# Kernel optimization log

Hardware: AMD Instinct MI355X
Metric: run time of the kernel (lower is better)

Reference implementation:

```python
import jax, jax.numpy as jnp
import numpy as np

SCALE_SIZE = 1.0
EPS = 1e-5
B, N, C, OUT, W = 32, 4096, 256, 512, 64


def _conv1x1(x, w, b):
    # x: (B, Cin, N), w: (Cout, Cin), b: (Cout,)
    return jnp.einsum('oc,bcn->bon', w, x) + b[:, None]


def _bn(x, g, be, m, v):
    # eval-mode BatchNorm1d over channel dim of (B, C, N)
    return (x - m[:, None]) * (g[:, None] / jnp.sqrt(v[:, None] + EPS)) + be[:, None]


def _bn_params(k, c):
    k1, k2, k3, k4 = jax.random.split(k, 4)
    g = jax.random.uniform(k1, (c,)) * 0.5 + 0.75
    be = jax.random.normal(k2, (c,)) * 0.1
    m = jax.random.normal(k3, (c,)) * 0.1
    v = jax.random.uniform(k4, (c,)) * 0.5 + 0.5
    return g, be, m, v


def setup_inputs() -> dict:
    key = jax.random.key(0)
    ks = jax.random.split(key, 16)
    d = {}
    d['xyz'] = jax.random.normal(ks[0], (B, N, 3), dtype=jnp.float32)
    d['feature'] = jax.random.normal(ks[1], (B, C, N), dtype=jnp.float32)
    d['idx'] = jax.random.randint(ks[2], (B, N), 0, N, dtype=jnp.int64)
    # WeightNet1D: 3 -> 64 -> 64 -> 64
    d['w1'] = jax.random.normal(ks[3], (W, 3), dtype=jnp.float32) * 0.3
    d['b1'] = jax.random.normal(ks[4], (W,), dtype=jnp.float32) * 0.05
    d['g1'], d['be1'], d['m1'], d['v1'] = _bn_params(ks[5], W)
    d['w2'] = jax.random.normal(ks[6], (W, W), dtype=jnp.float32) * 0.1
    d['b2'] = jax.random.normal(ks[7], (W,), dtype=jnp.float32) * 0.05
    d['g2'], d['be2'], d['m2'], d['v2'] = _bn_params(ks[8], W)
    d['w3'] = jax.random.normal(ks[9], (W, W), dtype=jnp.float32) * 0.1
    d['b3'] = jax.random.normal(ks[10], (W,), dtype=jnp.float32) * 0.05
    d['g3'], d['be3'], d['m3'], d['v3'] = _bn_params(ks[11], W)
    # final ConvBNRelu1D: C*W -> OUT, kernel 1
    d['wf'] = jax.random.normal(ks[12], (OUT, C * W), dtype=jnp.float32) * 0.01
    d['bf'] = jax.random.normal(ks[13], (OUT,), dtype=jnp.float32) * 0.05
    d['gf'], d['bef'], d['mf'], d['vf'] = _bn_params(ks[14], OUT)
    return d


def reference(xyz, feature, idx,
              w1, b1, g1, be1, m1, v1,
              w2, b2, g2, be2, m2, v2,
              w3, b3, g3, be3, m3, v3,
              wf, bf, gf, bef, mf, vf):
    # xyz: (B, N, 3) -> (B, 3, N), scaled
    x = jnp.transpose(xyz, (0, 2, 1)) / SCALE_SIZE
    x = jax.nn.relu(_bn(_conv1x1(x, w1, b1), g1, be1, m1, v1))
    x = jax.nn.relu(_bn(_conv1x1(x, w2, b2), g2, be2, m2, v2))
    weights = jax.nn.relu(_bn(_conv1x1(x, w3, b3), g3, be3, m3, v3))
    n = feature.shape[2]
    feat = feature / n
    # (B, C, N) x (B, N, 64) -> (B, C, 64)
    agg = jnp.einsum('bcn,bwn->bcw', feat, weights)
    agg = agg.reshape(agg.shape[0], -1, 1)  # (B, C*64, 1)
    out = jax.nn.relu(_bn(_conv1x1(agg, wf, bf), gf, bef, mf, vf))
    return out  # (B, OUT, 1)
```

## Files before the change

### kernel.cpp

```cpp
#include <hip/hip_runtime.h>
#include <hip/hip_bf16.h>

#define B_ 32
#define N_ 4096
#define C_ 256
#define W_ 64
#define OUT_ 512
#define EPS_ 1e-5f

typedef __attribute__((ext_vector_type(8))) short short8;
typedef __attribute__((ext_vector_type(4))) float floatx4;

#define WT_OFF     0
#define AGGB_OFF   16777216
#define PART_OFF   17825792
#define WS_NEEDED  19922944

#define GLOAD_LDS16(g, l)                                                  \
  __builtin_amdgcn_global_load_lds(                                        \
      (const __attribute__((address_space(1))) void*)(g),                  \
      (__attribute__((address_space(3))) void*)(l), 16, 0, 0)

__device__ __forceinline__ ushort f2bf(float f) {
  unsigned u = __builtin_bit_cast(unsigned, f);
  unsigned r = (u + 0x7fffu + ((u >> 16) & 1u)) >> 16;
  return (ushort)r;
}
__device__ __forceinline__ unsigned pk2(float a, float b) {
  return (unsigned)f2bf(a) | ((unsigned)f2bf(b) << 16);
}

__global__ __launch_bounds__(256) void k1_weightnet(
    const float* __restrict__ xyz,
    const float* __restrict__ w1, const float* __restrict__ b1,
    const float* __restrict__ g1, const float* __restrict__ be1,
    const float* __restrict__ m1, const float* __restrict__ v1,
    const float* __restrict__ w2, const float* __restrict__ b2,
    const float* __restrict__ g2, const float* __restrict__ be2,
    const float* __restrict__ m2, const float* __restrict__ v2,
    const float* __restrict__ w3, const float* __restrict__ b3,
    const float* __restrict__ g3, const float* __restrict__ be3,
    const float* __restrict__ m3, const float* __restrict__ v3,
    ushort* __restrict__ wt) {
  __shared__ __align__(16) ushort h_lds[256 * 72];
  __shared__ __align__(16) ushort w2_lds[64 * 72];
  __shared__ __align__(16) ushort w3_lds[64 * 72];
  __shared__ float w1l[192];
  __shared__ float b1l[64];
  __shared__ float b2_lds[64];
  __shared__ float b3_lds[64];

  const int t = threadIdx.x;
  const int blk = blockIdx.x;
  const int b = blk >> 4;
  const int n0 = (blk & 15) << 8;

  if (t < 64) {
    float s1 = g1[t] * rsqrtf(v1[t] + EPS_);
#pragma unroll
    for (int j = 0; j < 3; ++j) w1l[t * 3 + j] = w1[t * 3 + j] * s1;
    b1l[t] = (b1[t] - m1[t]) * s1 + be1[t];

    float s2 = g2[t] * rsqrtf(v2[t] + EPS_);
    unsigned* w2row = (unsigned*)&w2_lds[t * 72];
#pragma unroll
    for (int q = 0; q < 16; ++q) {
      float4 v = *(const float4*)&w2[t * 64 + q * 4];
      w2row[q * 2] = pk2(v.x * s2, v.y * s2);
      w2row[q * 2 + 1] = pk2(v.z * s2, v.w * s2);
    }
    w2row[32] = 0; w2row[33] = 0; w2row[34] = 0; w2row[35] = 0;
    b2_lds[t] = (b2[t] - m2[t]) * s2 + be2[t];

    float s3 = g3[t] * rsqrtf(v3[t] + EPS_);
    unsigned* w3row = (unsigned*)&w3_lds[t * 72];
#pragma unroll
    for (int q = 0; q < 16; ++q) {
      float4 v = *(const float4*)&w3[t * 64 + q * 4];
      w3row[q * 2] = pk2(v.x * s3, v.y * s3);
      w3row[q * 2 + 1] = pk2(v.z * s3, v.w * s3);
    }
    w3row[32] = 0; w3row[33] = 0; w3row[34] = 0; w3row[35] = 0;
    b3_lds[t] = (b3[t] - m3[t]) * s3 + be3[t];
  }
  __syncthreads();

  const int n = n0 + t;
  const float* xp = xyz + ((size_t)b * N_ + n) * 3;
  float x0 = xp[0], x1 = xp[1], x2 = xp[2];
  unsigned* hrow = (unsigned*)&h_lds[t * 72];
#pragma unroll 4
  for (int cp = 0; cp < 32; ++cp) {
    int c0 = cp * 2, c1 = cp * 2 + 1;
    float a0 = fmaxf(b1l[c0] + w1l[c0 * 3] * x0 + w1l[c0 * 3 + 1] * x1 + w1l[c0 * 3 + 2] * x2, 0.f);
    float a1 = fmaxf(b1l[c1] + w1l[c1 * 3] * x0 + w1l[c1 * 3 + 1] * x1 + w1l[c1 * 3 + 2] * x2, 0.f);
    hrow[cp] = pk2(a0, a1);
  }
  __syncthreads();

  const int wv = t >> 6, lane = t & 63;
  const int lrow = lane & 15, lk = lane >> 4;

  floatx4 acc[4][4];
#pragma unroll
  for (int mt = 0; mt < 4; ++mt)
#pragma unroll
    for (int nt = 0; nt < 4; ++nt) acc[mt][nt] = (floatx4){0.f, 0.f, 0.f, 0.f};

#pragma unroll
  for (int ks = 0; ks < 2; ++ks) {
    short8 afr[4], bfr[4];
#pragma unroll
    for (int mt = 0; mt < 4; ++mt)
      afr[mt] = *(const short8*)&h_lds[(wv * 64 + mt * 16 + lrow) * 72 + ks * 32 + lk * 8];
#pragma unroll
    for (int nt = 0; nt < 4; ++nt)
      bfr[nt] = *(const short8*)&w2_lds[(nt * 16 + lrow) * 72 + ks * 32 + lk * 8];
#pragma unroll
    for (int mt = 0; mt < 4; ++mt)
#pragma unroll
      for (int nt = 0; nt < 4; ++nt)
        acc[mt][nt] = __builtin_amdgcn_mfma_f32_16x16x32_bf16(afr[mt], bfr[nt], acc[mt][nt], 0, 0, 0);
  }
#pragma unroll
  for (int mt = 0; mt < 4; ++mt)
#pragma unroll
    for (int nt = 0; nt < 4; ++nt) {
      float bias = b2_lds[nt * 16 + lrow];
#pragma unroll
      for (int r = 0; r < 4; ++r) {
        float v = fmaxf(acc[mt][nt][r] + bias, 0.f);
        h_lds[(wv * 64 + mt * 16 + lk * 4 + r) * 72 + nt * 16 + lrow] = f2bf(v);
      }
    }

  floatx4 acc3[4][4];
#pragma unroll
  for (int mt = 0; mt < 4; ++mt)
#pragma unroll
    for (int nt = 0; nt < 4; ++nt) acc3[mt][nt] = (floatx4){0.f, 0.f, 0.f, 0.f};

#pragma unroll
  for (int ks = 0; ks < 2; ++ks) {
    short8 afr[4], bfr[4];
#pragma unroll
    for (int mt = 0; mt < 4; ++mt)
      afr[mt] = *(const short8*)&h_lds[(wv * 64 + mt * 16 + lrow) * 72 + ks * 32 + lk * 8];
#pragma unroll
    for (int nt = 0; nt < 4; ++nt)
      bfr[nt] = *(const short8*)&w3_lds[(nt * 16 + lrow) * 72 + ks * 32 + lk * 8];
#pragma unroll
    for (int mt = 0; mt < 4; ++mt)
#pragma unroll
      for (int nt = 0; nt < 4; ++nt)
        acc3[mt][nt] = __builtin_amdgcn_mfma_f32_16x16x32_bf16(afr[mt], bfr[nt], acc3[mt][nt], 0, 0, 0);
  }

  __syncthreads();
  unsigned* T = (unsigned*)h_lds;
#pragma unroll
  for (int mt = 0; mt < 4; ++mt)
#pragma unroll
    for (int nt = 0; nt < 4; ++nt) {
      float bias = b3_lds[nt * 16 + lrow];
      float v0 = fmaxf(acc3[mt][nt][0] + bias, 0.f);
      float v1 = fmaxf(acc3[mt][nt][1] + bias, 0.f);
      float v2 = fmaxf(acc3[mt][nt][2] + bias, 0.f);
      float v3 = fmaxf(acc3[mt][nt][3] + bias, 0.f);
      int ch = nt * 16 + lrow;
      int pp = (wv * 64 + mt * 16 + lk * 4) >> 1;
      T[ch * 132 + pp] = pk2(v0, v1);
      T[ch * 132 + pp + 1] = pk2(v2, v3);
    }
  __syncthreads();

  const int ch = t >> 2, q = t & 3;
  unsigned* wtu = (unsigned*)wt;
  size_t obase = ((size_t)(b * W_ + ch)) * (N_ / 2) + (n0 >> 1);
#pragma unroll
  for (int j = 0; j < 8; ++j) {
    int col = q * 4 + j * 16;
    uint4 vv = *(const uint4*)&T[ch * 132 + col];
    *(uint4*)&wtu[obase + col] = vv;
  }
}

__global__ __launch_bounds__(256) void k2_agg(const float* __restrict__ feature,
                                              const ushort* __restrict__ wt,
                                              ushort* __restrict__ aggB) {
  __shared__ __align__(16) float A_lds[3][32 * 128];
  __shared__ __align__(16) ushort B_lds[3][64 * 128];

  const int t = threadIdx.x;
  const int wv = t >> 6, lane = t & 63;
  const int lrow = lane & 15, lk = lane >> 4;
  const int blk = blockIdx.x;
  const int b = blk & 31;
  const int ct = blk >> 5;

  const float* fbase = feature + (size_t)(b * C_ + ct * 32) * N_;
  const ushort* wbase = wt + (size_t)(b * W_) * N_;

  const int rowA = (lane >> 5);
  const int colA = (lane & 31);
  const int rowB = (lane >> 4);
  const int colB = (lane & 15);

#define STAGE(buf, step)                                                          \
  do {                                                                            \
    _Pragma("unroll")                                                             \
    for (int q = 0; q < 4; ++q) {                                                 \
      int j = wv * 4 + q;                                                         \
      int ra = 2 * j + rowA;                                                      \
      int ga = colA ^ (ra & 7);              \
      GLOAD_LDS16(fbase + (size_t)ra * N_ + (step) * 128 + ga * 4,                \
                  &A_lds[buf][j * 256 + lane * 4]);                               \
      int rb = 4 * j + rowB;                                                      \
      int gb = colB ^ (rb & 7);                                                   \
      GLOAD_LDS16(wbase + (size_t)rb * N_ + (step) * 128 + gb * 8,                \
                  &B_lds[buf][j * 512 + lane * 8]);                               \
    }                                                                             \
  } while (0)

  const int cg = wv >> 1, wg = wv & 1;
  const int r_c = cg * 16 + lrow;
  const int eA = r_c & 7;
  const int r_w0 = wg * 32 + lrow;
  const int eB0 = r_w0 & 7, eB1 = (r_w0 + 16) & 7;

  floatx4 acc[2];
  acc[0] = (floatx4){0.f, 0.f, 0.f, 0.f};
  acc[1] = (floatx4){0.f, 0.f, 0.f, 0.f};

  auto compute = [&](int cur) {
    const float* abuf = &A_lds[cur][r_c * 128];
    const ushort* bbuf0 = &B_lds[cur][r_w0 * 128];
    const ushort* bbuf1 = &B_lds[cur][(r_w0 + 16) * 128];
#pragma unroll
    for (int ksl = 0; ksl < 4; ++ksl) {
      const int p = ksl * 8 + lk * 2;
      float4 fa = *(const float4*)&abuf[((p) ^ eA) * 4];
      float4 fb = *(const float4*)&abuf[((p + 1) ^ eA) * 4];
      union { unsigned u[4]; short8 s8; } pa;
      pa.u[0] = pk2(fa.x, fa.y);
      pa.u[1] = pk2(fa.z, fa.w);
      pa.u[2] = pk2(fb.x, fb.y);
      pa.u[3] = pk2(fb.z, fb.w);
      const int g = ksl * 4 + lk;
      short8 b0 = *(const short8*)&bbuf0[(g ^ eB0) * 8];
      short8 b1 = *(const short8*)&bbuf1[(g ^ eB1) * 8];
      acc[0] = __builtin_amdgcn_mfma_f32_16x16x32_bf16(pa.s8, b0, acc[0], 0, 0, 0);
      acc[1] = __builtin_amdgcn_mfma_f32_16x16x32_bf16(pa.s8, b1, acc[1], 0, 0, 0);
    }
  };

#define WAIT_BAR(n) asm volatile("s_waitcnt vmcnt(" #n ")\n\ts_barrier" ::: "memory")
#define BAR()       asm volatile("s_barrier" ::: "memory")

  STAGE(0, 0);
  STAGE(1, 1);
  for (int g = 0; g < 10; ++g) {
    STAGE(2, 3 * g + 2); WAIT_BAR(16); compute(0); BAR();
    STAGE(0, 3 * g + 3); WAIT_BAR(16); compute(1); BAR();
    STAGE(1, 3 * g + 4); WAIT_BAR(16); compute(2); BAR();
  }
  WAIT_BAR(8);  compute(0); BAR();
  WAIT_BAR(0);  compute(1);
#undef STAGE
#undef WAIT_BAR
#undef BAR

  const float sc = 1.f / 4096.f;
  ushort* dst = aggB + (size_t)b * 16384;
#pragma unroll
  for (int wt2 = 0; wt2 < 2; ++wt2)
#pragma unroll
    for (int r = 0; r < 4; ++r) {
      int c = ct * 32 + cg * 16 + lk * 4 + r;
      int w = wg * 32 + wt2 * 16 + lrow;
      dst[c * 64 + w] = f2bf(acc[wt2][r] * sc);
    }
}

__global__ __launch_bounds__(256) void k3_final(const float* __restrict__ wf,
                                                const ushort* __restrict__ aggB,
                                                float* __restrict__ part) {
  const int t = threadIdx.x;
  const int wv = t >> 6, lane = t & 63;
  const int lrow = lane & 15, lk = lane >> 4;
  const int ot = blockIdx.x >> 5;
  const int kb = blockIdx.x & 31;
  const int o0 = ot * 64 + wv * 16;
  const int k0 = kb * 512;

  const float* wp = wf + (size_t)(o0 + lrow) * 16384 + k0 + lk * 8;
  const ushort* a0 = aggB + (size_t)lrow * 16384 + k0 + lk * 8;
  const ushort* a1 = a0 + (size_t)16 * 16384;

  floatx4 acc0 = {0.f, 0.f, 0.f, 0.f}, acc1 = {0.f, 0.f, 0.f, 0.f};
#pragma unroll 8
  for (int s = 0; s < 16; ++s) {
    float4 f0 = *(const float4*)(wp + s * 32);
    float4 f1 = *(const float4*)(wp + s * 32 + 4);
    short8 b0 = *(const short8*)(a0 + s * 32);
    short8 b1 = *(const short8*)(a1 + s * 32);
    union { unsigned u[4]; short8 s8; } pa;
    pa.u[0] = pk2(f0.x, f0.y);
    pa.u[1] = pk2(f0.z, f0.w);
    pa.u[2] = pk2(f1.x, f1.y);
    pa.u[3] = pk2(f1.z, f1.w);
    acc0 = __builtin_amdgcn_mfma_f32_16x16x32_bf16(pa.s8, b0, acc0, 0, 0, 0);
    acc1 = __builtin_amdgcn_mfma_f32_16x16x32_bf16(pa.s8, b1, acc1, 0, 0, 0);
  }

  float* dst = part + (size_t)kb * 16384;
#pragma unroll
  for (int r = 0; r < 4; ++r) {
    int o = o0 + lk * 4 + r;
    dst[o * 32 + lrow] = acc0[r];
    dst[o * 32 + 16 + lrow] = acc1[r];
  }
}

__global__ __launch_bounds__(64) void k4_finalize(
    const float* __restrict__ bf, const float* __restrict__ gf,
    const float* __restrict__ bef, const float* __restrict__ mf,
    const float* __restrict__ vf, const float* __restrict__ part,
    float* __restrict__ out) {
  int i = blockIdx.x * 64 + threadIdx.x;
  int o = i >> 5, b = i & 31;
  float v = 0.f;
#pragma unroll
  for (int kb = 0; kb < 32; ++kb) v += part[(size_t)kb * 16384 + i];
  float s = gf[o] * rsqrtf(vf[o] + EPS_);
  float r = (v + bf[o] - mf[o]) * s + bef[o];
  out[b * OUT_ + o] = fmaxf(r, 0.f);
}

extern "C" void kernel_launch(void* const* d_in, const int* in_sizes, int n_in,
                              void* d_out, int out_size, void* d_ws, size_t ws_size,
                              hipStream_t stream) {
  const float* xyz     = (const float*)d_in[0];
  const float* feature = (const float*)d_in[1];
  const float* w1 = (const float*)d_in[3];
  const float* b1 = (const float*)d_in[4];
  const float* g1 = (const float*)d_in[5];
  const float* be1 = (const float*)d_in[6];
  const float* m1 = (const float*)d_in[7];
  const float* v1 = (const float*)d_in[8];
  const float* w2 = (const float*)d_in[9];
  const float* b2 = (const float*)d_in[10];
  const float* g2 = (const float*)d_in[11];
  const float* be2 = (const float*)d_in[12];
  const float* m2 = (const float*)d_in[13];
  const float* v2 = (const float*)d_in[14];
  const float* w3 = (const float*)d_in[15];
  const float* b3 = (const float*)d_in[16];
  const float* g3 = (const float*)d_in[17];
  const float* be3 = (const float*)d_in[18];
  const float* m3 = (const float*)d_in[19];
  const float* v3 = (const float*)d_in[20];
  const float* wf = (const float*)d_in[21];
  const float* bf = (const float*)d_in[22];
  const float* gf = (const float*)d_in[23];
  const float* bef = (const float*)d_in[24];
  const float* mf = (const float*)d_in[25];
  const float* vf = (const float*)d_in[26];

  char* ws = (char*)d_ws;
  if (ws_size < (size_t)WS_NEEDED) return;
  ushort* wt   = (ushort*)(ws + WT_OFF);
  ushort* aggB = (ushort*)(ws + AGGB_OFF);
  float*  part = (float*)(ws + PART_OFF);

  k1_weightnet<<<512, 256, 0, stream>>>(xyz,
                                        w1, b1, g1, be1, m1, v1,
                                        w2, b2, g2, be2, m2, v2,
                                        w3, b3, g3, be3, m3, v3, wt);
  k2_agg<<<256, 256, 0, stream>>>(feature, wt, aggB);
  k3_final<<<256, 256, 0, stream>>>(wf, aggB, part);
  k4_finalize<<<256, 64, 0, stream>>>(bf, gf, bef, mf, vf, part, (float*)d_out);
}
```

Measured before the change: 61.22 us.

## Convert feature to bf16 in registers before LDS and double-buffer agg kernel

The aggregation kernel now loads feature rows into registers, converts them to bf16 with a cheaper round-half-up pack, and writes them to LDS in swizzled form. Previously it copied fp32 rows straight into LDS and converted on every MFMA read. The K step grows from 128 to 256 and the pipeline drops from triple to double buffering with a full wait per step. This halves LDS footprint and read traffic for A and removes repeated conversion work. The trade-offs are higher register use and less overlap, because each step waits on vmcnt(0). The final GEMV kernel also switches to the cheaper pk2h rounding, which rounds ties away from zero instead of to nearest even.

```diff
diff --git a/kernel.cpp b/kernel.cpp
--- a/kernel.cpp
+++ b/kernel.cpp
@@ -28,6 +28,11 @@
 }
 __device__ __forceinline__ unsigned pk2(float a, float b) {
   return (unsigned)f2bf(a) | ((unsigned)f2bf(b) << 16);
+}
+__device__ __forceinline__ unsigned pk2h(float a, float b) {
+  unsigned ua = __builtin_bit_cast(unsigned, a);
+  unsigned ub = __builtin_bit_cast(unsigned, b);
+  return ((ua + 0x8000u) >> 16) | ((ub + 0x8000u) & 0xffff0000u);
 }
 
 __global__ __launch_bounds__(256) void k1_weightnet(
@@ -188,98 +193,118 @@
 __global__ __launch_bounds__(256) void k2_agg(const float* __restrict__ feature,
                                               const ushort* __restrict__ wt,
                                               ushort* __restrict__ aggB) {
-  __shared__ __align__(16) float A_lds[3][32 * 128];
-  __shared__ __align__(16) ushort B_lds[3][64 * 128];
+  __shared__ __align__(16) ushort A_lds[2][32 * 256];
+  __shared__ __align__(16) ushort B_lds[2][64 * 256];
 
   const int t = threadIdx.x;
   const int wv = t >> 6, lane = t & 63;
   const int lrow = lane & 15, lk = lane >> 4;
-  const int blk = blockIdx.x;
-  const int b = blk & 31;
-  const int ct = blk >> 5;
+  const int b = blockIdx.x & 31;
+  const int ct = blockIdx.x >> 5;
 
   const float* fbase = feature + (size_t)(b * C_ + ct * 32) * N_;
   const ushort* wbase = wt + (size_t)(b * W_) * N_;
 
-  const int rowA = (lane >> 5);
-  const int colA = (lane & 31);
-  const int rowB = (lane >> 4);
-  const int colB = (lane & 15);
-
-#define STAGE(buf, step)                                                          \
-  do {                                                                            \
-    _Pragma("unroll")                                                             \
-    for (int q = 0; q < 4; ++q) {                                                 \
-      int j = wv * 4 + q;                                                         \
-      int ra = 2 * j + rowA;                                                      \
-      int ga = colA ^ (ra & 7);              \
-      GLOAD_LDS16(fbase + (size_t)ra * N_ + (step) * 128 + ga * 4,                \
-                  &A_lds[buf][j * 256 + lane * 4]);                               \
-      int rb = 4 * j + rowB;                                                      \
-      int gb = colB ^ (rb & 7);                                                   \
-      GLOAD_LDS16(wbase + (size_t)rb * N_ + (step) * 128 + gb * 8,                \
-                  &B_lds[buf][j * 512 + lane * 8]);                               \
-    }                                                                             \
+  const int aj = wv * 8 + (lane >> 3);
+  const int ac = (lane & 7) * 32;
+  const float* fsrc = fbase + (size_t)aj * N_ + ac;
+  const int eAW = aj & 7;
+
+  const int brh = lane >> 5;
+  const int bgr = lane & 31;
+
+  float4 areg[8];
+
+#define A_ISSUE(step)                                                        \
+  do {                                                                       \
+    _Pragma("unroll")                                                        \
+    for (int q = 0; q < 8; ++q)                                              \
+      areg[q] = *(const float4*)(fsrc + (size_t)(step) * 256 + q * 4);       \
   } while (0)
 
+#define A_WRITE(buf)                                                         \
+  do {                                                                       \
+    ushort* drow = &A_lds[buf][aj * 256];                                    \
+    _Pragma("unroll")                                                        \
+    for (int w = 0; w < 4; ++w) {                                            \
+      uint4 d;                                                               \
+      d.x = pk2h(areg[w * 2].x, areg[w * 2].y);                              \
+      d.y = pk2h(areg[w * 2].z, areg[w * 2].w);                              \
+      d.z = pk2h(areg[w * 2 + 1].x, areg[w * 2 + 1].y);                      \
+      d.w = pk2h(areg[w * 2 + 1].z, areg[w * 2 + 1].w);                      \
+      int g = ((lane & 7) * 4 + w) ^ eAW;                                    \
+      *(uint4*)(drow + g * 8) = d;                                           \
+    }                                                                        \
+  } while (0)
+
+#define B_STAGE(buf, step)                                                   \
+  do {                                                                       \
+    _Pragma("unroll")                                                        \
+    for (int j2 = 0; j2 < 8; ++j2) {                                         \
+      int row = wv * 16 + 2 * j2 + brh;                                      \
+      int sg = bgr ^ (row & 7);                                              \
+      GLOAD_LDS16(wbase + (size_t)row * N_ + (step) * 256 + sg * 8,          \
+                  &B_lds[buf][(wv * 16 + 2 * j2) * 256 + lane * 8]);         \
+    }                                                                        \
+  } while (0)
+
   const int cg = wv >> 1, wg = wv & 1;
-  const int r_c = cg * 16 + lrow;
-  const int eA = r_c & 7;
-  const int r_w0 = wg * 32 + lrow;
-  const int eB0 = r_w0 & 7, eB1 = (r_w0 + 16) & 7;
-
-  floatx4 acc[2];
-  acc[0] = (floatx4){0.f, 0.f, 0.f, 0.f};
-  acc[1] = (floatx4){0.f, 0.f, 0.f, 0.f};
-
-  auto compute = [&](int cur) {
-    const float* abuf = &A_lds[cur][r_c * 128];
-    const ushort* bbuf0 = &B_lds[cur][r_w0 * 128];
-    const ushort* bbuf1 = &B_lds[cur][(r_w0 + 16) * 128];
-#pragma unroll
-    for (int ksl = 0; ksl < 4; ++ksl) {
-      const int p = ksl * 8 + lk * 2;
-      float4 fa = *(const float4*)&abuf[((p) ^ eA) * 4];
-      float4 fb = *(const float4*)&abuf[((p + 1) ^ eA) * 4];
-      union { unsigned u[4]; short8 s8; } pa;
-      pa.u[0] = pk2(fa.x, fa.y);
-      pa.u[1] = pk2(fa.z, fa.w);
-      pa.u[2] = pk2(fb.x, fb.y);
-      pa.u[3] = pk2(fb.z, fb.w);
-      const int g = ksl * 4 + lk;
-      short8 b0 = *(const short8*)&bbuf0[(g ^ eB0) * 8];
-      short8 b1 = *(const short8*)&bbuf1[(g ^ eB1) * 8];
-      acc[0] = __builtin_amdgcn_mfma_f32_16x16x32_bf16(pa.s8, b0, acc[0], 0, 0, 0);
-      acc[1] = __builtin_amdgcn_mfma_f32_16x16x32_bf16(pa.s8, b1, acc[1], 0, 0, 0);
-    }
-  };
-
-#define WAIT_BAR(n) asm volatile("s_waitcnt vmcnt(" #n ")\n\ts_barrier" ::: "memory")
-#define BAR()       asm volatile("s_barrier" ::: "memory")
-
-  STAGE(0, 0);
-  STAGE(1, 1);
-  for (int g = 0; g < 10; ++g) {
-    STAGE(2, 3 * g + 2); WAIT_BAR(16); compute(0); BAR();
-    STAGE(0, 3 * g + 3); WAIT_BAR(16); compute(1); BAR();
-    STAGE(1, 3 * g + 4); WAIT_BAR(16); compute(2); BAR();
-  }
-  WAIT_BAR(8);  compute(0); BAR();
-  WAIT_BAR(0);  compute(1);
-#undef STAGE
-#undef WAIT_BAR
-#undef BAR
+  const int rA = cg * 16 + lrow, eA = rA & 7;
+  const int rB0 = wg * 32 + lrow, eB0 = rB0 & 7;
+  const int rB1 = rB0 + 16, eB1 = rB1 & 7;
+
+  floatx4 acc0 = {0.f, 0.f, 0.f, 0.f}, acc1 = {0.f, 0.f, 0.f, 0.f};
+
+#define COMPUTE(buf)                                                         \
+  do {                                                                       \
+    const ushort* Ab = &A_lds[buf][rA * 256];                                \
+    const ushort* Bb0 = &B_lds[buf][rB0 * 256];                              \
+    const ushort* Bb1 = &B_lds[buf][rB1 * 256];                              \
+    _Pragma("unroll")                                                        \
+    for (int ksl = 0; ksl < 8; ++ksl) {                                      \
+      int g = ksl * 4 + lk;                                                  \
+      short8 a = *(const short8*)(Ab + (g ^ eA) * 8);                        \
+      short8 b0 = *(const short8*)(Bb0 + (g ^ eB0) * 8);                     \
+      short8 b1 = *(const short8*)(Bb1 + (g ^ eB1) * 8);                     \
+      acc0 = __builtin_amdgcn_mfma_f32_16x16x32_bf16(a, b0, acc0, 0, 0, 0);  \
+      acc1 = __builtin_amdgcn_mfma_f32_16x16x32_bf16(a, b1, acc1, 0, 0, 0);  \
+    }                                                                        \
+  } while (0)
+
+#define SYNC_STEP() asm volatile("s_waitcnt vmcnt(0) lgkmcnt(0)\n\ts_barrier" ::: "memory")
+
+  A_ISSUE(0); B_STAGE(0, 0);
+  A_WRITE(0);
+  A_ISSUE(1); B_STAGE(1, 1);
+  asm volatile("s_waitcnt vmcnt(16) lgkmcnt(0)\n\ts_barrier" ::: "memory");
+
+#pragma unroll 2
+  for (int s = 0; s < 14; ++s) {
+    const int cur = s & 1;
+    COMPUTE(cur);
+    A_WRITE(cur ^ 1);
+    SYNC_STEP();
+    A_ISSUE(s + 2); B_STAGE(cur, s + 2);
+  }
+  COMPUTE(0);
+  A_WRITE(1);
+  SYNC_STEP();
+  COMPUTE(1);
+
+#undef A_ISSUE
+#undef A_WRITE
+#undef B_STAGE
+#undef COMPUTE
+#undef SYNC_STEP
 
   const float sc = 1.f / 4096.f;
   ushort* dst = aggB + (size_t)b * 16384;
 #pragma unroll
-  for (int wt2 = 0; wt2 < 2; ++wt2)
-#pragma unroll
-    for (int r = 0; r < 4; ++r) {
-      int c = ct * 32 + cg * 16 + lk * 4 + r;
-      int w = wg * 32 + wt2 * 16 + lrow;
-      dst[c * 64 + w] = f2bf(acc[wt2][r] * sc);
-    }
+  for (int r = 0; r < 4; ++r) {
+    int c = ct * 32 + cg * 16 + lk * 4 + r;
+    dst[c * 64 + wg * 32 + lrow] = f2bf(acc0[r] * sc);
+    dst[c * 64 + wg * 32 + 16 + lrow] = f2bf(acc1[r] * sc);
+  }
 }
 
 __global__ __launch_bounds__(256) void k3_final(const float* __restrict__ wf,
@@ -305,10 +330,10 @@
     short8 b0 = *(const short8*)(a0 + s * 32);
     short8 b1 = *(const short8*)(a1 + s * 32);
     union { unsigned u[4]; short8 s8; } pa;
-    pa.u[0] = pk2(f0.x, f0.y);
-    pa.u[1] = pk2(f0.z, f0.w);
-    pa.u[2] = pk2(f1.x, f1.y);
-    pa.u[3] = pk2(f1.z, f1.w);
+    pa.u[0] = pk2h(f0.x, f0.y);
+    pa.u[1] = pk2h(f0.z, f0.w);
+    pa.u[2] = pk2h(f1.x, f1.y);
+    pa.u[3] = pk2h(f1.z, f1.w);
     acc0 = __builtin_amdgcn_mfma_f32_16x16x32_bf16(pa.s8, b0, acc0, 0, 0, 0);
     acc1 = __builtin_amdgcn_mfma_f32_16x16x32_bf16(pa.s8, b1, acc1, 0, 0, 0);
   }
```

Result: slower. 70.62 us (+15.3%).
